# Kernel optimization log

Measured on AMD Instinct MI355X. Metric: run time of the kernel, lower is better.

## Reference

```python
import jax, jax.numpy as jnp
import numpy as np

GAMMA_MIN = 1e-4
BIG = 1e9  # stands in for +inf; exp(-BIG/gamma) == 0 exactly in fp32, avoids inf-inf NaNs
M, N, D = 4096, 4096, 512


def setup_inputs() -> dict:
    key = jax.random.key(0)
    k1, k2 = jax.random.split(key)
    x = jax.random.normal(k1, (M, D), dtype=jnp.float32)
    y = jax.random.normal(k2, (N, D), dtype=jnp.float32)
    gamma = jnp.asarray(1.0, dtype=jnp.float32)
    return {"x": x, "y": y, "gamma": gamma}


def _softmin(stacked, gamma):
    # softmin over axis 0: -gamma * logsumexp(-v / gamma)
    return -gamma * jax.nn.logsumexp(-stacked / gamma, axis=0)


def _forward_dp(cost, gamma):
    # Anti-diagonal wavefront. diag_d[i] = R[i, d - i] with R (m+1, n+1) DP, R[0,0]=0.
    m, n = cost.shape
    idx = jnp.arange(m + 1)
    diag0 = jnp.full((m + 1,), BIG, cost.dtype).at[0].set(0.0)  # d = 0
    diag1 = jnp.full((m + 1,), BIG, cost.dtype)                 # d = 1 (boundary = inf)

    def step(carry, d):
        prev2, prev1 = carry  # diag_{d-2}, diag_{d-1}
        j = d - idx
        valid = (idx >= 1) & (j >= 1) & (j <= n)
        c = cost[jnp.clip(idx - 1, 0, m - 1), jnp.clip(j - 1, 0, n - 1)]
        p2 = jnp.roll(prev2, 1).at[0].set(BIG)  # R[i-1, j-1]
        p1 = jnp.roll(prev1, 1).at[0].set(BIG)  # R[i-1, j]
        new = jnp.where(valid, c + _softmin(jnp.stack([p2, p1, prev1]), gamma), BIG)
        return (prev1, new), new

    _, diags = jax.lax.scan(step, (diag0, diag1), jnp.arange(2, m + n + 1))
    ii = jnp.arange(1, m + 1)[:, None]
    jj = jnp.arange(1, n + 1)[None, :]
    return diags[ii + jj - 2, ii]  # (m, n): dp_f at cell (i, j)


def _backward_dp(cost, gamma):
    # Reverse DP: E[m,n] = 0; E[i,j] = softmin over reachable successors + cost.
    m, n = cost.shape
    idx = jnp.arange(m + 1)
    diag_top = jnp.full((m + 1,), BIG, cost.dtype)               # d = m+n+1
    diag_mn = jnp.full((m + 1,), BIG, cost.dtype).at[m].set(0.0)  # d = m+n

    def cost_at(i0, j0):
        return cost[jnp.clip(i0, 0, m - 1), jnp.clip(j0, 0, n - 1)]

    def step(carry, d):
        nxt1, nxt2 = carry  # diag_{d+1}, diag_{d+2}
        j = d - idx
        valid = (idx >= 1) & (j >= 1) & (j <= n)
        n1 = jnp.roll(nxt1, -1).at[m].set(BIG)  # E[i+1, j]
        n2 = jnp.roll(nxt2, -1).at[m].set(BIG)  # E[i+1, j+1]
        ok1 = valid & (idx <= m - 1) & (j <= n - 1)
        ok2 = valid & (idx <= m - 1)
        ok3 = valid & (j <= n - 1)
        c1 = jnp.where(ok1, n2 + cost_at(idx, j), BIG)        # diag move
        c2 = jnp.where(ok2, n1 + cost_at(idx, j - 1), BIG)    # down move
        c3 = jnp.where(ok3, nxt1 + cost_at(idx - 1, j), BIG)  # right move
        new = jnp.where(valid, _softmin(jnp.stack([c1, c2, c3]), gamma), BIG)
        new = jnp.where((idx == m) & (j == n), 0.0, new)  # (m,n) stays 0
        return (new, nxt1), new

    _, diags = jax.lax.scan(step, (diag_mn, diag_top), jnp.arange(m + n - 1, 1, -1))
    diags_all = jnp.concatenate([diag_mn[None, :], diags], axis=0)  # row k holds d = m+n-k
    ii = jnp.arange(1, m + 1)[:, None]
    jj = jnp.arange(1, n + 1)[None, :]
    return diags_all[m + n - ii - jj, ii]  # (m, n)


def reference(x, y, gamma):
    g = jnp.maximum(jnp.abs(gamma), GAMMA_MIN)
    xn = x / jnp.maximum(jnp.linalg.norm(x, axis=-1, keepdims=True), 1e-12)
    yn = y / jnp.maximum(jnp.linalg.norm(y, axis=-1, keepdims=True), 1e-12)
    cost = 1.0 - xn @ yn.T  # (M, N) cosine distance
    dp_f = _forward_dp(cost, g)
    distance = dp_f[-1, -1]
    dp_b = _backward_dp(cost, g)
    log_p = jnp.minimum(-(dp_f + cost + dp_b - distance) / g, 0.0)
    alignment = jnp.exp(log_p)
    total = jnp.maximum(alignment.sum(), 1e-8)
    alignment = alignment / total * min(cost.shape)
    return alignment, distance
```

## Files before the change

kernel.cpp:

```cpp
#include <hip/hip_runtime.h>
#include <stdint.h>

#define MDIM 4096
#define NDIM 4096
#define DDIM 512
#define BIGV 1e9f
#define GAMMA_MIN 1e-4f

#define CH 32
#define NSTEPS (NDIM + 63)
#define NCHUNK ((NSTEPS + CH - 1) / CH)
#define CLO 2
#define CHI 127
#define WPB 4
#define NBR 16
#define NDPB (2 * NBR)
#define NHEAT 224

#define LOG2E_F 1.4426950408889634f
#define LN2_F   0.69314718055994531f
#define TAGBASE 0x5A5A0000u

__device__ __forceinline__ float f4c(const float4 v, int j) {
  switch (j & 3) { case 0: return v.x; case 1: return v.y; case 2: return v.z; default: return v.w; }
}
__device__ __forceinline__ float4 ld4u(const float* p) { return *(const float4*)p; }
typedef float f4a __attribute__((ext_vector_type(4), aligned(4)));
__device__ __forceinline__ void st4u(float* p, float a, float b, float c, float d) {
  f4a v = {a, b, c, d};
  *(f4a*)p = v;
}
__device__ __forceinline__ float wshr1o(float old, float x) {
  int r = __builtin_amdgcn_update_dpp(__builtin_bit_cast(int, old),
                                      __builtin_bit_cast(int, x), 0x138, 0xF, 0xF, false);
  return __builtin_bit_cast(float, r);
}
__device__ __forceinline__ uint64_t haloLoad1(const uint64_t* hbase, int col0, int lane) {
  int idx = col0 + (lane & 15);
  if (idx > NDIM - 1) idx = NDIM - 1;
  return __hip_atomic_load(hbase + idx, __ATOMIC_RELAXED, __HIP_MEMORY_SCOPE_AGENT);
}
__device__ __forceinline__ uint64_t haloSpin(const uint64_t* hbase, int col0, int lane,
                                             uint64_t cur) {
  int idx = col0 + (lane & 15);
  if (idx > NDIM - 1) idx = NDIM - 1;
  const uint32_t etag = TAGBASE | (uint32_t)idx;
  while (__ballot((uint32_t)(cur >> 32) == etag) != ~0ull) {
    __builtin_amdgcn_s_sleep(1);
    cur = __hip_atomic_load(hbase + idx, __ATOMIC_RELAXED, __HIP_MEMORY_SCOPE_AGENT);
  }
  return cur;
}
__device__ __forceinline__ void haloUnpack2(uint64_t w0, uint64_t w1, float* hA) {
  const int lo0 = (int)(uint32_t)(w0 & 0xFFFFFFFFull);
  const int lo1 = (int)(uint32_t)(w1 & 0xFFFFFFFFull);
#pragma unroll
  for (int s = 0; s < 16; ++s) {
    hA[s]      = __builtin_bit_cast(float, __builtin_amdgcn_readlane(lo0, s));
    hA[16 + s] = __builtin_bit_cast(float, __builtin_amdgcn_readlane(lo1, s));
  }
}
__device__ __forceinline__ void haloStore(uint64_t* hbase, int col, float v) {
  const uint64_t u = ((uint64_t)(TAGBASE | (uint32_t)col) << 32) |
                     (uint64_t)__builtin_bit_cast(uint32_t, v);
  __hip_atomic_store(hbase + col, u, __ATOMIC_RELAXED, __HIP_MEMORY_SCOPE_AGENT);
}
__device__ __forceinline__ int ldsFlagLoad(const int* p) {
  return __hip_atomic_load(p, __ATOMIC_RELAXED, __HIP_MEMORY_SCOPE_WORKGROUP);
}
__device__ __forceinline__ void ldsFlagStore(int* p, int v) {
  __hip_atomic_store(p, v, __ATOMIC_RELAXED, __HIP_MEMORY_SCOPE_WORKGROUP);
}

__global__ void init_small(double* __restrict__ sum_p, float* __restrict__ dist_p,
                           int* __restrict__ done_p) {
  if (threadIdx.x == 0) *sum_p = 0.0;
  if (threadIdx.x == 1) *dist_p = 0.0f;
  if (threadIdx.x == 2) *done_p = 0;
}

__global__ __launch_bounds__(128) void norm_rows(const float* __restrict__ x,
                                                 const float* __restrict__ y,
                                                 float* __restrict__ xn,
                                                 float* __restrict__ yn) {
  const int row = blockIdx.x;
  const float* src = (row < MDIM) ? (x + (size_t)row * DDIM) : (y + (size_t)(row - MDIM) * DDIM);
  float*       dst = (row < MDIM) ? (xn + (size_t)row * DDIM) : (yn + (size_t)(row - MDIM) * DDIM);
  float4 v = ((const float4*)src)[threadIdx.x];
  float ss = v.x * v.x + v.y * v.y + v.z * v.z + v.w * v.w;
#pragma unroll
  for (int off = 32; off > 0; off >>= 1) ss += __shfl_down(ss, off);
  __shared__ float acc[2];
  if ((threadIdx.x & 63) == 0) acc[threadIdx.x >> 6] = ss;
  __syncthreads();
  const float total = acc[0] + acc[1];
  const float inv = 1.0f / fmaxf(sqrtf(total), 1e-12f);
  v.x *= inv; v.y *= inv; v.z *= inv; v.w *= inv;
  ((float4*)dst)[threadIdx.x] = v;
}

#define GT 128
__global__ __launch_bounds__(256) void gemm_cost(const float* __restrict__ xn,
                                                 const float* __restrict__ yn,
                                                 float* __restrict__ cost) {
  __shared__ float As[16][GT + 4];
  __shared__ float Bs[16][GT + 4];
  const int t  = threadIdx.x;
  const int bx = blockIdx.x & 31;
  const int by = blockIdx.x >> 5;
  const int tx = t & 15, ty = t >> 4;
  const int lrow = t >> 1;
  const int lk   = (t & 1) * 8;
  const float* arow = xn + (size_t)(by * GT + lrow) * DDIM + lk;
  const float* brow = yn + (size_t)(bx * GT + lrow) * DDIM + lk;

  float acc[8][8];
#pragma unroll
  for (int i = 0; i < 8; ++i)
#pragma unroll
    for (int j = 0; j < 8; ++j) acc[i][j] = 0.0f;

  for (int kt = 0; kt < DDIM; kt += 16) {
    const float4 a0 = *(const float4*)(arow + kt);
    const float4 a1 = *(const float4*)(arow + kt + 4);
    const float4 b0 = *(const float4*)(brow + kt);
    const float4 b1 = *(const float4*)(brow + kt + 4);
    __syncthreads();
    As[lk + 0][lrow] = a0.x; As[lk + 1][lrow] = a0.y; As[lk + 2][lrow] = a0.z; As[lk + 3][lrow] = a0.w;
    As[lk + 4][lrow] = a1.x; As[lk + 5][lrow] = a1.y; As[lk + 6][lrow] = a1.z; As[lk + 7][lrow] = a1.w;
    Bs[lk + 0][lrow] = b0.x; Bs[lk + 1][lrow] = b0.y; Bs[lk + 2][lrow] = b0.z; Bs[lk + 3][lrow] = b0.w;
    Bs[lk + 4][lrow] = b1.x; Bs[lk + 5][lrow] = b1.y; Bs[lk + 6][lrow] = b1.z; Bs[lk + 7][lrow] = b1.w;
    __syncthreads();
#pragma unroll
    for (int k = 0; k < 16; ++k) {
      const float4 av0 = *(const float4*)&As[k][ty * 8];
      const float4 av1 = *(const float4*)&As[k][ty * 8 + 4];
      const float4 bv0 = *(const float4*)&Bs[k][tx * 8];
      const float4 bv1 = *(const float4*)&Bs[k][tx * 8 + 4];
      const float av[8] = {av0.x, av0.y, av0.z, av0.w, av1.x, av1.y, av1.z, av1.w};
      const float bv[8] = {bv0.x, bv0.y, bv0.z, bv0.w, bv1.x, bv1.y, bv1.z, bv1.w};
#pragma unroll
      for (int i = 0; i < 8; ++i)
#pragma unroll
        for (int j = 0; j < 8; ++j) acc[i][j] = fmaf(av[i], bv[j], acc[i][j]);
    }
  }
#pragma unroll
  for (int i = 0; i < 8; ++i) {
    const size_t row = (size_t)(by * GT + ty * 8 + i);
    float* o = cost + row * NDIM + bx * GT + tx * 8;
    const float4 o0 = make_float4(1.0f - acc[i][0], 1.0f - acc[i][1], 1.0f - acc[i][2], 1.0f - acc[i][3]);
    const float4 o1 = make_float4(1.0f - acc[i][4], 1.0f - acc[i][5], 1.0f - acc[i][6], 1.0f - acc[i][7]);
    *(float4*)o = o0;
    *(float4*)(o + 4) = o1;
  }
}

template <int DIR>
__device__ void run_band(const float* __restrict__ cost, float* __restrict__ dpOut,
                         uint64_t* __restrict__ halo, float* dist_out, float g,
                         int br, int w, int lane,
                         float* lhaloR, float* lhaloW, int* flagR, int* flagW) {
  const float k1 = LOG2E_F / g;
  const float k2 = g * LN2_F;
  const int b = br * WPB + w;
  const int r = b * 64 + lane;
  const float* crow = DIR ? (cost + (size_t)(MDIM - 1 - r) * NDIM + (NDIM - 1))
                          : (cost + (size_t)r * NDIM);
  float* myrow = dpOut + (size_t)r * NDIM;
  const bool top   = (b == 0);
  const bool ldsR  = (w > 0);
  const bool globR = (!top && !ldsR);
  const bool ldsW  = (w < WPB - 1);
  const bool globW = (!ldsW && br < NBR - 1);
  const uint64_t* ghR = halo + (size_t)(DIR * NBR + (br > 0 ? br - 1 : 0)) * NDIM;
  uint64_t*       ghW = halo + (size_t)(DIR * NBR + br) * NDIM;

  float v_prev = BIGV;
  float w2 = (top && lane == 0) ? 0.0f : BIGV;
  float vk  = v_prev * k1;
  float w2k = w2 * k1;

  float4 cc[8], cn1[8], cn2[8];
#pragma unroll
  for (int q = 0; q < 8; ++q) {
    const int cb0 = 0 * CH - lane, cb1 = 1 * CH - lane, cb2 = 2 * CH - lane;
    cc[q]  = DIR ? ld4u(crow - cb0 - 4 * q - 3) : ld4u(crow + cb0 + 4 * q);
    cn1[q] = DIR ? ld4u(crow - cb1 - 4 * q - 3) : ld4u(crow + cb1 + 4 * q);
    cn2[q] = DIR ? ld4u(crow - cb2 - 4 * q - 3) : ld4u(crow + cb2 + 4 * q);
  }

  float hA[CH];
  uint64_t hB0 = 0, hB1 = 0, hC0 = 0, hC1 = 0;
  if (globR) {
    uint64_t h0 = haloLoad1(ghR, 0, lane);
    h0 = haloSpin(ghR, 0, lane, h0);
    uint64_t h1 = haloLoad1(ghR, 16, lane);
    h1 = haloSpin(ghR, 16, lane, h1);
    haloUnpack2(h0, h1, hA);
    hB0 = haloLoad1(ghR, 1 * CH, lane);
    hB1 = haloLoad1(ghR, 1 * CH + 16, lane);
    hC0 = haloLoad1(ghR, 2 * CH, lane);
    hC1 = haloLoad1(ghR, 2 * CH + 16, lane);
  } else if (ldsR) {
    while (ldsFlagLoad(flagR) < 3) __builtin_amdgcn_s_sleep(1);
    asm volatile("" ::: "memory");
    const float4* lp = (const float4*)&lhaloR[0];
#pragma unroll
    for (int q = 0; q < 8; ++q) {
      const float4 hv = lp[q];
      hA[4 * q] = hv.x; hA[4 * q + 1] = hv.y; hA[4 * q + 2] = hv.z; hA[4 * q + 3] = hv.w;
    }
  }

  for (int c = 0; c < NCHUNK; ++c) {
    float buf[CH];
    const int t0 = c * CH;
    const int base = t0 - lane;
    if (c >= CLO && c <= CHI) {
#pragma unroll
      for (int s = 0; s < CH; ++s) {
        const float hold = top ? BIGV : hA[s];
        const float w1 = wshr1o(hold, v_prev);
        const float w1k = w1 * k1;
        const float m = fminf(fminf(w2, w1), v_prev);
        const float e = exp2f(fmaf(m, k1, -w2k)) + exp2f(fmaf(m, k1, -w1k)) +
                        exp2f(fmaf(m, k1, -vk));
        const float cval = DIR ? f4c(cc[s >> 2], 3 - (s & 3)) : f4c(cc[s >> 2], s);
        const float v = fmaf(-k2, log2f(e), m + cval);
        buf[s] = v;
        v_prev = v; vk = v * k1;
        w2 = w1; w2k = w1k;
      }
    } else {
#pragma unroll
      for (int s = 0; s < CH; ++s) {
        const float hold = top ? BIGV : hA[s];
        const float w1 = wshr1o(hold, v_prev);
        const float w1k = w1 * k1;
        const float m = fminf(fminf(w2, w1), v_prev);
        const float e = exp2f(fmaf(m, k1, -w2k)) + exp2f(fmaf(m, k1, -w1k)) +
                        exp2f(fmaf(m, k1, -vk));
        const float cval = DIR ? f4c(cc[s >> 2], 3 - (s & 3)) : f4c(cc[s >> 2], s);
        const float v = fmaf(-k2, log2f(e), m + cval);
        buf[s] = v;
        const bool act = (base + s >= 0) && (base + s < NDIM);
        v_prev = act ? v : v_prev;
        vk     = act ? v * k1 : vk;
        w2 = w1; w2k = w1k;
      }
    }

    if (globR && c + 1 <= NDIM / CH) {
      hB0 = haloSpin(ghR, CH * (c + 1), lane, hB0);
      hB1 = haloSpin(ghR, CH * (c + 1) + 16, lane, hB1);
      haloUnpack2(hB0, hB1, hA);
      hB0 = hC0; hB1 = hC1;
      hC0 = haloLoad1(ghR, CH * (c + 3), lane);
      hC1 = haloLoad1(ghR, CH * (c + 3) + 16, lane);
    } else if (ldsR && c + 1 <= CHI) {
      int need = c + 4;
      if (need > NCHUNK) need = NCHUNK;
      while (ldsFlagLoad(flagR) < need) __builtin_amdgcn_s_sleep(1);
      asm volatile("" ::: "memory");
      const float4* lp = (const float4*)&lhaloR[CH * (c + 1)];
#pragma unroll
      for (int q = 0; q < 8; ++q) {
        const float4 hv = lp[q];
        hA[4 * q] = hv.x; hA[4 * q + 1] = hv.y; hA[4 * q + 2] = hv.z; hA[4 * q + 3] = hv.w;
      }
    }

#pragma unroll
    for (int q = 0; q < 8; ++q) { cc[q] = cn1[q]; cn1[q] = cn2[q]; }
    {
      const int cb = (c + 3) * CH - lane;
#pragma unroll
      for (int q = 0; q < 8; ++q)
        cn2[q] = DIR ? ld4u(crow - cb - 4 * q - 3) : ld4u(crow + cb + 4 * q);
    }

    if (c >= CLO && c <= CHI) {
#pragma unroll
      for (int q = 0; q < 8; ++q)
        st4u(myrow + base + 4 * q, buf[4 * q], buf[4 * q + 1], buf[4 * q + 2], buf[4 * q + 3]);
    } else {
#pragma unroll
      for (int s = 0; s < CH; ++s) {
        const int col = base + s;
        if (col >= 0 && col < NDIM) myrow[col] = buf[s];
      }
    }
    if (ldsW) {
      if (lane == 63) {
        if (c >= CLO && c <= CHI) {
#pragma unroll
          for (int s = 0; s < CH; ++s) lhaloW[base + s] = buf[s];
        } else {
#pragma unroll
          for (int s = 0; s < CH; ++s) {
            const int col = base + s;
            if (col >= 0 && col < NDIM) lhaloW[col] = buf[s];
          }
        }
      }
      asm volatile("s_waitcnt lgkmcnt(0)" ::: "memory");
      if (lane == 63) ldsFlagStore(flagW, c + 1);
    } else if (globW && lane == 63) {
      if (c >= CLO && c <= CHI) {
#pragma unroll
        for (int s = 0; s < CH; ++s) haloStore(ghW, base + s, buf[s]);
      } else {
#pragma unroll
        for (int s = 0; s < CH; ++s) {
          const int col = base + s;
          if (col >= 0 && col < NDIM) haloStore(ghW, col, buf[s]);
        }
      }
    }
  }
  if (DIR == 0 && b == 63 && lane == 63) *dist_out = v_prev;
}

__global__ __launch_bounds__(256, 1) void dp_kernel(const float* __restrict__ cost,
                                                    float* __restrict__ dpF, float* __restrict__ dpG,
                                                    uint64_t* __restrict__ halo, float* dist_out,
                                                    const float* __restrict__ gamma_p,
                                                    int* __restrict__ done_p) {
  if (blockIdx.x >= NDPB) {
    float t0 = (float)threadIdx.x + 1.0f, t1 = t0 + 0.5f, t2 = t0 + 0.25f, t3 = t0 + 0.125f;
    int off = (int)(blockIdx.x * 1031 + threadIdx.x);
    while (__hip_atomic_load(done_p, __ATOMIC_RELAXED, __HIP_MEMORY_SCOPE_AGENT) < NDPB) {
#pragma unroll 8
      for (int i = 0; i < 256; ++i) {
        t0 = fmaf(t0, 1.0000001f, 0.03125f);
        t1 = fmaf(t1, 0.9999999f, 0.03125f);
        t2 = fmaf(t2, 1.0000002f, 0.03125f);
        t3 = fmaf(t3, 0.9999998f, 0.03125f);
      }
      off = (off + 4099) & (MDIM * NDIM - 1);
      t0 = fmaf(cost[off], 1e-30f, t0);
    }
    if (t0 + t1 + t2 + t3 == -1.0f && threadIdx.x == 12345) *done_p = 99;
    return;
  }
  __shared__ float lh[WPB - 1][NDIM];
  __shared__ int   lf[WPB - 1];
  const int w = threadIdx.x >> 6, lane = threadIdx.x & 63;
  if (threadIdx.x < WPB - 1) lf[threadIdx.x] = 0;
  __syncthreads();
  const int dir = blockIdx.x >> 4;
  const int br  = blockIdx.x & 15;
  const float g = fmaxf(fabsf(gamma_p[0]), GAMMA_MIN);
  float* lhR = (w > 0) ? lh[w - 1] : nullptr;
  float* lhW = (w < WPB - 1) ? lh[w] : nullptr;
  int* fR = (w > 0) ? &lf[w - 1] : nullptr;
  int* fW = (w < WPB - 1) ? &lf[w] : nullptr;
  if (dir == 0) run_band<0>(cost, dpF, halo, dist_out, g, br, w, lane, lhR, lhW, fR, fW);
  else          run_band<1>(cost, dpG, halo, dist_out, g, br, w, lane, lhR, lhW, fR, fW);
  __syncthreads();
  if (threadIdx.x == 0)
    __hip_atomic_fetch_add(done_p, 1, __ATOMIC_RELAXED, __HIP_MEMORY_SCOPE_AGENT);
}

__global__ __launch_bounds__(256) void pass1(float* __restrict__ out, const float* __restrict__ dpG,
                                             const float* __restrict__ dist_p,
                                             const float* __restrict__ gamma_p,
                                             double* __restrict__ sum_p) {
  const size_t idx4 = (size_t)blockIdx.x * 256 + threadIdx.x;
  const size_t base = idx4 * 4;
  const float g = fmaxf(fabsf(gamma_p[0]), GAMMA_MIN);
  const float invg = 1.0f / g;
  const float dist = *dist_p;
  const float4 f = ((const float4*)out)[idx4];
  const float4 grev = ((const float4*)dpG)[(16777212u - base) >> 2];
  const float x0 = fminf((dist - f.x - grev.w) * invg, 0.0f);
  const float x1 = fminf((dist - f.y - grev.z) * invg, 0.0f);
  const float x2 = fminf((dist - f.z - grev.y) * invg, 0.0f);
  const float x3 = fminf((dist - f.w - grev.x) * invg, 0.0f);
  const float a0 = exp2f(x0 * LOG2E_F), a1 = exp2f(x1 * LOG2E_F);
  const float a2 = exp2f(x2 * LOG2E_F), a3 = exp2f(x3 * LOG2E_F);
  ((float4*)out)[idx4] = make_float4(a0, a1, a2, a3);
  float s = a0 + a1 + a2 + a3;
#pragma unroll
  for (int off = 32; off > 0; off >>= 1) s += __shfl_down(s, off);
  __shared__ float wsum[4];
  if ((threadIdx.x & 63) == 0) wsum[threadIdx.x >> 6] = s;
  __syncthreads();
  if (threadIdx.x == 0) atomicAdd(sum_p, (double)(wsum[0] + wsum[1] + wsum[2] + wsum[3]));
}

__global__ __launch_bounds__(256) void pass2(float* __restrict__ out,
                                             const double* __restrict__ sum_p,
                                             const float* __restrict__ dist_p) {
  const size_t idx4 = (size_t)blockIdx.x * 256 + threadIdx.x;
  const float total = fmaxf((float)*sum_p, 1e-8f);
  const float scale = 4096.0f / total;
  float4 v = ((const float4*)out)[idx4];
  v.x *= scale; v.y *= scale; v.z *= scale; v.w *= scale;
  ((float4*)out)[idx4] = v;
  if (idx4 == 0) out[16777216] = *dist_p;
}

extern "C" void kernel_launch(void* const* d_in, const int* in_sizes, int n_in,
                              void* d_out, int out_size, void* d_ws, size_t ws_size,
                              hipStream_t stream) {
  const float* x = (const float*)d_in[0];
  const float* y = (const float*)d_in[1];
  const float* gamma_p = (const float*)d_in[2];
  float* out = (float*)d_out;

  uint8_t* w = (uint8_t*)d_ws;
  const size_t SZ_MAT = (size_t)MDIM * NDIM * sizeof(float);
  const size_t SZ_XN  = (size_t)MDIM * DDIM * sizeof(float);
  float* xn  = (float*)w;
  float* yn  = (float*)(w + SZ_XN);
  float* dpG = (float*)w;
  float* cost = (float*)(w + SZ_MAT + 512);
  uint8_t* small = w + SZ_MAT + 512 + SZ_MAT + 512;
  double* sum_p  = (double*)small;
  float*  dist_p = (float*)(small + 8);
  int*    done_p = (int*)(small + 16);
  uint64_t* halo = (uint64_t*)d_in[0];

  hipLaunchKernelGGL(init_small, dim3(1), dim3(64), 0, stream, sum_p, dist_p, done_p);
  hipLaunchKernelGGL(norm_rows, dim3(2 * MDIM), dim3(128), 0, stream, x, y, xn, yn);
  hipLaunchKernelGGL(gemm_cost, dim3((MDIM / GT) * (NDIM / GT)), dim3(256), 0, stream, xn, yn, cost);
  hipLaunchKernelGGL(dp_kernel, dim3(NDPB + NHEAT), dim3(64 * WPB), 0, stream,
                     cost, out, dpG, halo, dist_p, gamma_p, done_p);
  hipLaunchKernelGGL(pass1, dim3(MDIM * NDIM / 1024), dim3(256), 0, stream, out, dpG, dist_p, gamma_p, sum_p);
  hipLaunchKernelGGL(pass2, dim3(MDIM * NDIM / 1024), dim3(256), 0, stream, out, sum_p, dist_p);
}
```

Measured before the change: 2.054 ms.

## Run interior soft-DTW recurrence in scaled exponential domain instead of log domain

For interior chunks, the soft-min recurrence is carried in probability space (P = exp(-v/gamma)) with per-lane exponent renormalisation and double-precision log offsets. This replaces three exp2 plus one log2 per cell with multiply-adds, one exp2 for the cost kernel and one for the halo term. Log-domain values are rebuilt for output and at the chunk-range boundary. The risks are extra shuffle and bit-manipulation overhead, double arithmetic, and numerical precision or underflow issues from the rescaling.

Result: no change. 2.057 ms (+0.1%).

```diff
diff --git a/kernel.cpp b/kernel.cpp
--- a/kernel.cpp
+++ b/kernel.cpp
@@ -180,6 +180,9 @@
   float w2 = (top && lane == 0) ? 0.0f : BIGV;
   float vk  = v_prev * k1;
   float w2k = w2 * k1;
+  float P_l = 0.0f, P_d = 0.0f;
+  double Btot = 0.0;
+  const float beta = exp2f(k1);
 
   float4 cc[8], cn1[8], cn2[8];
 #pragma unroll
@@ -218,21 +221,64 @@
     const int t0 = c * CH;
     const int base = t0 - lane;
     if (c >= CLO && c <= CHI) {
-#pragma unroll
-      for (int s = 0; s < CH; ++s) {
-        const float hold = top ? BIGV : hA[s];
-        const float w1 = wshr1o(hold, v_prev);
-        const float w1k = w1 * k1;
-        const float m = fminf(fminf(w2, w1), v_prev);
-        const float e = exp2f(fmaf(m, k1, -w2k)) + exp2f(fmaf(m, k1, -w1k)) +
-                        exp2f(fmaf(m, k1, -vk));
-        const float cval = DIR ? f4c(cc[s >> 2], 3 - (s & 3)) : f4c(cc[s >> 2], s);
-        const float v = fmaf(-k2, log2f(e), m + cval);
-        buf[s] = v;
-        v_prev = v; vk = v * k1;
-        w2 = w1; w2k = w1k;
-      }
+      const double Tc0d = (double)(b * 64 + t0);
+      if (c == CLO) {
+        Btot = (double)v_prev - (Tc0d - 1.0);
+        P_l  = 1.0f;
+        P_d  = exp2f((v_prev - 1.0f - w2) * k1);
+      } else {
+        const int mb = __builtin_bit_cast(int, P_l);
+        int E = ((mb >> 23) & 0xFF) - 127;
+        E = E < -120 ? -120 : (E > 120 ? 120 : E);
+        const float rho = __builtin_bit_cast(float, (127 - E) << 23);
+        P_l *= rho; P_d *= rho;
+        Btot -= (double)k2 * (double)E;
+      }
+      const double BtU = __shfl_up(Btot, 1);
+      float fup = exp2f((float)(Btot - BtU) * k1);
+      const float vbf = (float)(Tc0d + Btot);
+      const double Bt0 = __shfl(Btot, 0);
+      const float hcf = (float)(Tc0d - 1.0 + Bt0);
+      int Ecum = 0, E0cum = 0;
+#pragma unroll
+      for (int qs = 0; qs < 8; ++qs) {
+        if (qs) {
+          const int mb2 = __builtin_bit_cast(int, P_l);
+          int E = ((mb2 >> 23) & 0xFF) - 127;
+          E = E < -120 ? -120 : (E > 120 ? 120 : E);
+          const float rho = __builtin_bit_cast(float, (127 - E) << 23);
+          int dE = __shfl_up(E, 1) - E;
+          dE = dE < -120 ? -120 : (dE > 120 ? 120 : dE);
+          const float fsc = __builtin_bit_cast(float, (127 + dE) << 23);
+          const int E0 = __shfl(E, 0);
+          P_l *= rho; P_d *= rho; fup *= fsc;
+          Ecum += E; E0cum += E0;
+        }
+        const float Ecf = (float)Ecum;
+        const float E0f = (float)E0cum;
+#pragma unroll
+        for (int si = 0; si < 4; ++si) {
+          const int s = qs * 4 + si;
+          const float targ = hcf + (float)s - hA[s];
+          const float hps = top ? 0.0f : exp2f(fmaf(targ, k1, -E0f));
+          const float Pu = wshr1o(hps, P_l) * fup;
+          float S = Pu + P_l;
+          S = fmaf(beta, P_d, S);
+          const float cval = DIR ? f4c(cc[s >> 2], 3 - (s & 3)) : f4c(cc[s >> 2], s);
+          const float Kv = exp2f(fmaf(-cval, k1, k1));
+          const float P = Kv * S;
+          buf[s] = fminf(fmaxf(fmaf(-k2, log2f(P) + Ecf, vbf + (float)s), -BIGV), BIGV);
+          P_d = Pu; P_l = P;
+        }
+      }
+      Btot -= (double)k2 * (double)Ecum;
     } else {
+      if (c == CHI + 1) {
+        const double TcBd = (double)(b * 64 + t0);
+        v_prev = fminf(fmaf(-k2, log2f(P_l), (float)(TcBd - 1.0 + Btot)), BIGV);
+        w2     = fminf(fmaf(-k2, log2f(P_d), (float)(TcBd - 2.0 + Btot)), BIGV);
+        vk = v_prev * k1; w2k = w2 * k1;
+      }
 #pragma unroll
       for (int s = 0; s < CH; ++s) {
         const float hold = top ? BIGV : hA[s];
```
